# Optimization experiments

Measured on AMD Instinct MI355X. Metric: run time of the kernel, lower is better.

Reference implementation:

```python
import jax, jax.numpy as jnp
import numpy as np

N, E, G = 100000, 1600000, 64   # nodes, edges, graphs
IN, H, OUT = 32, 128, 3


def setup_inputs() -> dict:
    key = jax.random.key(0)
    ks = jax.random.split(key, 24)
    def w(k, i, o):
        return (jax.random.normal(k, (i, o), jnp.float32) / np.sqrt(i)).astype(jnp.float32)
    inp = {
        "x": jax.random.normal(ks[0], (N, IN), jnp.float32),
        "edge_index": jax.random.randint(ks[1], (2, E), 0, N, dtype=jnp.int32).astype(jnp.int64),
        "batch": jnp.sort(jax.random.randint(ks[2], (N,), 0, G, dtype=jnp.int32)).astype(jnp.int64),
        # SAGEConv layer 0 (in->hidden): lin_l (neighbors, with bias), lin_r (root, no bias)
        "Wl0": w(ks[3], IN, H), "bl0": jnp.zeros((H,), jnp.float32), "Wr0": w(ks[4], IN, H),
        # SAGEConv layers 1,2 (hidden->hidden)
        "Wl1": w(ks[5], H, H), "bl1": jnp.zeros((H,), jnp.float32), "Wr1": w(ks[6], H, H),
        "Wl2": w(ks[7], H, H), "bl2": jnp.zeros((H,), jnp.float32), "Wr2": w(ks[8], H, H),
        # output head
        "Wfc": w(ks[9], H, OUT), "bfc": jnp.zeros((OUT,), jnp.float32),
        # aux MLP on (dim1, dim3)
        "Wa1": w(ks[10], 2, H), "ba1": jnp.zeros((H,), jnp.float32),
        "Wa2": w(ks[11], H, H), "ba2": jnp.zeros((H,), jnp.float32),
        "Wao": w(ks[12], H, 1), "bao": jnp.zeros((1,), jnp.float32),
    }
    return inp


def _sage_conv(x, src, dst, Wl, bl, Wr):
    # PyG SAGEConv (mean aggr): out = lin_l(mean_{j in N(i)} x_j) + lin_r(x_i)
    msg = x[src]                                   # [E, d] gather
    agg = jax.ops.segment_sum(msg, dst, num_segments=N)
    cnt = jax.ops.segment_sum(jnp.ones((src.shape[0],), x.dtype), dst, num_segments=N)
    mean = agg / jnp.maximum(cnt, 1.0)[:, None]
    return mean @ Wl + bl + x @ Wr


def reference(x, edge_index, batch,
              Wl0, bl0, Wr0, Wl1, bl1, Wr1, Wl2, bl2, Wr2,
              Wfc, bfc, Wa1, ba1, Wa2, ba2, Wao, bao):
    src, dst = edge_index[0], edge_index[1]
    h = jax.nn.relu(_sage_conv(x, src, dst, Wl0, bl0, Wr0))   # dropout is identity in eval
    h = jax.nn.relu(_sage_conv(h, src, dst, Wl1, bl1, Wr1))
    h = jax.nn.relu(_sage_conv(h, src, dst, Wl2, bl2, Wr2))
    main = h @ Wfc + bfc                                      # [N, 3]
    dim1, dim3 = main[:, 0], main[:, 2]
    aux_in = jnp.stack([dim1, dim3], axis=-1)                 # [N, 2]
    a = jax.nn.relu(aux_in @ Wa1 + ba1)
    a = jax.nn.relu(a @ Wa2 + ba2)
    aux_out = (a @ Wao + bao)[:, 0]                           # [N]
    final = jnp.stack([dim1, aux_out, dim3], axis=-1)         # [N, 3]
    # global mean pool over graph ids
    s = jax.ops.segment_sum(final, batch, num_segments=G)
    c = jax.ops.segment_sum(jnp.ones((final.shape[0],), final.dtype), batch, num_segments=G)
    return s / jnp.maximum(c, 1.0)[:, None]                   # [G, 3]
```

## Files before the change

kernel.cpp:

```cpp
#include <hip/hip_runtime.h>

#define NR 128
#define PART_CH 4096
typedef unsigned short ushortT;
typedef __attribute__((ext_vector_type(8))) short short8;
typedef __attribute__((ext_vector_type(4))) float float4v;
typedef __attribute__((ext_vector_type(2))) float float2v;

__device__ __forceinline__ unsigned short f32_to_bf16_rne(float f) {
    unsigned u = __float_as_uint(f);
    unsigned r = (u + 0x7fffu + ((u >> 16) & 1u)) >> 16;
    return (unsigned short)r;
}

__device__ __forceinline__ unsigned char f32_to_fp8(float f) {
    return (unsigned char)(__builtin_amdgcn_cvt_pk_fp8_f32(f, f, 0, false) & 0xff);
}

__device__ __forceinline__ void accum8(float* acc, uint4 v) {
    unsigned u[4] = {v.x, v.y, v.z, v.w};
#pragma unroll
    for (int q = 0; q < 4; q++) {
        acc[2 * q]     += __uint_as_float(u[q] << 16);
        acc[2 * q + 1] += __uint_as_float(u[q] & 0xffff0000u);
    }
}

__device__ __forceinline__ void accum16_fp8(float* acc, uint4 v) {
    unsigned u[4] = {v.x, v.y, v.z, v.w};
#pragma unroll
    for (int q = 0; q < 4; q++) {
        float2v lo = __builtin_amdgcn_cvt_pk_f32_fp8(u[q], false);
        float2v hi = __builtin_amdgcn_cvt_pk_f32_fp8(u[q], true);
        acc[4 * q + 0] += lo.x;
        acc[4 * q + 1] += lo.y;
        acc[4 * q + 2] += hi.x;
        acc[4 * q + 3] += hi.y;
    }
}


__launch_bounds__(256)
__global__ void bucket_count(const int* __restrict__ dst, int* __restrict__ bcnt, int E, int NB) {
    __shared__ int h[1024];
    int t = threadIdx.x;
    for (int j = t; j < NB; j += 256) h[j] = 0;
    __syncthreads();
    int e0 = blockIdx.x * PART_CH;
    int e1 = min(e0 + PART_CH, E);
    for (int base = e0; base < e1; base += 2048) {
        int idx = base + t;
        int d[8];
        int cnt = 0;
#pragma unroll
        for (int u = 0; u < 8; u++) {
            int e = idx + u * 256;
            if (e < e1) d[cnt++] = dst[e];
        }
        for (int u = 0; u < cnt; u++) atomicAdd(&h[d[u] >> 7], 1);
    }
    __syncthreads();
    for (int j = t; j < NB; j += 256) {
        int v = h[j];
        if (v) atomicAdd(&bcnt[j], v);
    }
}

__launch_bounds__(256)
__global__ void bucket_scan(const int* __restrict__ bcnt, int* __restrict__ bstart,
                            int* __restrict__ gcur, int NB, int E) {
    __shared__ int sh[256];
    int t = threadIdx.x;
    int v[4];
    int tot = 0;
#pragma unroll
    for (int j = 0; j < 4; j++) {
        int idx = t * 4 + j;
        v[j] = (idx < NB) ? bcnt[idx] : 0;
        tot += v[j];
    }
    sh[t] = tot;
    __syncthreads();
    for (int off = 1; off < 256; off <<= 1) {
        int add = (t >= off) ? sh[t - off] : 0;
        __syncthreads();
        sh[t] += add;
        __syncthreads();
    }
    int run = sh[t] - tot;
#pragma unroll
    for (int j = 0; j < 4; j++) {
        int idx = t * 4 + j;
        if (idx < NB) { bstart[idx] = run; gcur[idx] = run; }
        run += v[j];
    }
    if (t == 0) bstart[NB] = E;
}

__launch_bounds__(256)
__global__ void partition_edges(const int* __restrict__ src, const int* __restrict__ dst,
                                int* __restrict__ gcur, unsigned* __restrict__ packed,
                                int E, int NB) {
    __shared__ int hist[1024];
    __shared__ int base[1024];
    int t = threadIdx.x;
    int e0 = blockIdx.x * PART_CH;
    int e1 = min(e0 + PART_CH, E);
    for (int j = t; j < NB; j += 256) hist[j] = 0;
    __syncthreads();
    for (int bb = e0; bb < e1; bb += 2048) {
        int idx = bb + t;
        int d[8];
        int cnt = 0;
#pragma unroll
        for (int u = 0; u < 8; u++) {
            int e = idx + u * 256;
            if (e < e1) d[cnt++] = dst[e];
        }
        for (int u = 0; u < cnt; u++) atomicAdd(&hist[d[u] >> 7], 1);
    }
    __syncthreads();
    for (int j = t; j < NB; j += 256) {
        int h = hist[j];
        base[j] = h ? atomicAdd(&gcur[j], h) : 0;
    }
    __syncthreads();
    for (int j = t; j < NB; j += 256) hist[j] = base[j];
    __syncthreads();
    for (int bb = e0; bb < e1; bb += 2048) {
        int idx = bb + t;
        int d[8], s[8];
        int cnt = 0;
#pragma unroll
        for (int u = 0; u < 8; u++) {
            int e = idx + u * 256;
            if (e < e1) { d[cnt] = dst[e]; s[cnt] = src[e]; cnt++; }
        }
        for (int u = 0; u < cnt; u++) {
            int dd = d[u];
            int pos = atomicAdd(&hist[dd >> 7], 1);
            packed[pos] = (unsigned)s[u] | ((unsigned)(dd & (NR - 1)) << 17);
        }
    }
}

__launch_bounds__(256)
__global__ void bucket_sort(const unsigned* __restrict__ packed, const int* __restrict__ bstart,
                            int* __restrict__ row_start, int* __restrict__ srcs, int N) {
    __shared__ int cnt[NR];
    __shared__ int sc[NR];
    __shared__ int cur[NR];
    int b = blockIdx.x, t = threadIdx.x;
    int nb0 = b * NR;
    int nnode = min(NR, N - nb0);
    int lo = bstart[b], hi = bstart[b + 1];
    if (t < NR) cnt[t] = 0;
    __syncthreads();
    for (int bb = lo; bb < hi; bb += 2048) {
        int idx = bb + t;
        unsigned pk[8];
        int c = 0;
#pragma unroll
        for (int u = 0; u < 8; u++) {
            int e = idx + u * 256;
            if (e < hi) pk[c++] = packed[e];
        }
        for (int u = 0; u < c; u++) atomicAdd(&cnt[pk[u] >> 17], 1);
    }
    __syncthreads();
    if (t < NR) sc[t] = cnt[t];
    __syncthreads();
    for (int off = 1; off < NR; off <<= 1) {
        int add = (t >= off && t < NR) ? sc[t - off] : 0;
        __syncthreads();
        if (t < NR) sc[t] += add;
        __syncthreads();
    }
    if (t < nnode) {
        int s = lo + sc[t] - cnt[t];
        row_start[nb0 + t] = s;
        cur[t] = s;
    }
    if (t == 0 && nb0 + nnode == N) row_start[N] = hi;
    __syncthreads();
    for (int bb = lo; bb < hi; bb += 2048) {
        int idx = bb + t;
        unsigned pk[8];
        int c = 0;
#pragma unroll
        for (int u = 0; u < 8; u++) {
            int e = idx + u * 256;
            if (e < hi) pk[c++] = packed[e];
        }
        for (int u = 0; u < c; u++) {
            int pos = atomicAdd(&cur[pk[u] >> 17], 1);
            srcs[pos] = (int)(pk[u] & 0x1FFFFu);
        }
    }
}


__global__ void prep_fused(const float* __restrict__ x, ushortT* __restrict__ xbf, int n4,
                           const float* __restrict__ Wl0, const float* __restrict__ Wr0,
                           const float* __restrict__ Wl1, const float* __restrict__ Wr1,
                           const float* __restrict__ Wl2, const float* __restrict__ Wr2,
                           const float* __restrict__ Wa2,
                           ushortT* __restrict__ Wt0, ushortT* __restrict__ Wt1,
                           ushortT* __restrict__ Wt2, ushortT* __restrict__ Wa2t) {
    int tid0 = blockIdx.x * 256 + threadIdx.x;
    if (tid0 < n4) {
        float4 v = ((const float4*)x)[tid0];
        ushort4 o;
        o.x = f32_to_bf16_rne(v.x);
        o.y = f32_to_bf16_rne(v.y);
        o.z = f32_to_bf16_rne(v.z);
        o.w = f32_to_bf16_rne(v.w);
        ((ushort4*)xbf)[tid0] = o;
        return;
    }
    int tid = tid0 - n4;
    if (tid < 8192) {
        int col = tid >> 6, k = tid & 63;
        float v = (k < 32) ? Wl0[k * 128 + col] : Wr0[(k - 32) * 128 + col];
        Wt0[col * 64 + ((k + 8 * col) & 63)] = f32_to_bf16_rne(v);
    } else if (tid < 8192 + 32768) {
        int j = tid - 8192;
        int col = j >> 8, k = j & 255;
        float v = (k < 128) ? Wl1[k * 128 + col] : Wr1[(k - 128) * 128 + col];
        Wt1[col * 256 + ((k + 8 * col) & 255)] = f32_to_bf16_rne(v);
    } else if (tid < 8192 + 65536) {
        int j = tid - 8192 - 32768;
        int col = j >> 8, k = j & 255;
        float v = (k < 128) ? Wl2[k * 128 + col] : Wr2[(k - 128) * 128 + col];
        Wt2[col * 256 + ((k + 8 * col) & 255)] = f32_to_bf16_rne(v);
    } else if (tid < 8192 + 65536 + 16384) {
        int j = tid - 8192 - 65536;
        int col = j >> 7, k = j & 127;
        Wa2t[col * 128 + ((k + 8 * col) & 127)] = f32_to_bf16_rne(Wa2[k * 128 + col]);
    }
}


template <int CPN>
__launch_bounds__(256)
__global__ void aggregate_mean_bf16(const uint4* __restrict__ hin, ushortT* __restrict__ out,
                                    const int* __restrict__ srcs, const int* __restrict__ rs, int n) {
    constexpr int TPN = CPN / 2;
    int tid = blockIdx.x * 256 + threadIdx.x;
    if (tid >= n * TPN) return;
    int i = tid / TPN;
    int c = tid & (TPN - 1);
    int lo = rs[i], hi = rs[i + 1];
    float acc0[8], acc1[8];
#pragma unroll
    for (int q = 0; q < 8; q++) { acc0[q] = 0.f; acc1[q] = 0.f; }
    int e = lo;
    for (; e + 8 <= hi; e += 8) {
        int s[8];
#pragma unroll
        for (int u = 0; u < 8; u++) s[u] = srcs[e + u];
        uint4 va[8], vb[8];
#pragma unroll
        for (int u = 0; u < 8; u++) {
            va[u] = hin[(size_t)s[u] * CPN + c];
            vb[u] = hin[(size_t)s[u] * CPN + c + TPN];
        }
#pragma unroll
        for (int u = 0; u < 8; u++) { accum8(acc0, va[u]); accum8(acc1, vb[u]); }
    }
    for (; e < hi; ++e) {
        int s = srcs[e];
        accum8(acc0, hin[(size_t)s * CPN + c]);
        accum8(acc1, hin[(size_t)s * CPN + c + TPN]);
    }
    float inv = 1.0f / (float)max(hi - lo, 1);
    uint4 o0, o1;
    o0.x = (unsigned)f32_to_bf16_rne(acc0[0] * inv) | ((unsigned)f32_to_bf16_rne(acc0[1] * inv) << 16);
    o0.y = (unsigned)f32_to_bf16_rne(acc0[2] * inv) | ((unsigned)f32_to_bf16_rne(acc0[3] * inv) << 16);
    o0.z = (unsigned)f32_to_bf16_rne(acc0[4] * inv) | ((unsigned)f32_to_bf16_rne(acc0[5] * inv) << 16);
    o0.w = (unsigned)f32_to_bf16_rne(acc0[6] * inv) | ((unsigned)f32_to_bf16_rne(acc0[7] * inv) << 16);
    o1.x = (unsigned)f32_to_bf16_rne(acc1[0] * inv) | ((unsigned)f32_to_bf16_rne(acc1[1] * inv) << 16);
    o1.y = (unsigned)f32_to_bf16_rne(acc1[2] * inv) | ((unsigned)f32_to_bf16_rne(acc1[3] * inv) << 16);
    o1.z = (unsigned)f32_to_bf16_rne(acc1[4] * inv) | ((unsigned)f32_to_bf16_rne(acc1[5] * inv) << 16);
    o1.w = (unsigned)f32_to_bf16_rne(acc1[6] * inv) | ((unsigned)f32_to_bf16_rne(acc1[7] * inv) << 16);
    ((uint4*)out)[(size_t)i * CPN + c] = o0;
    ((uint4*)out)[(size_t)i * CPN + c + TPN] = o1;
}


__launch_bounds__(256)
__global__ void aggregate_mean_fp8(const uint4* __restrict__ hin, ushortT* __restrict__ out,
                                   const int* __restrict__ srcs, const int* __restrict__ rs, int n) {
    int tid = blockIdx.x * 256 + threadIdx.x;
    if (tid >= n * 8) return;
    int i = tid >> 3;
    int c = tid & 7;
    int lo = rs[i], hi = rs[i + 1];
    float acc[16];
#pragma unroll
    for (int q = 0; q < 16; q++) acc[q] = 0.f;
    int e = lo;
    for (; e + 8 <= hi; e += 8) {
        int s[8];
#pragma unroll
        for (int u = 0; u < 8; u++) s[u] = srcs[e + u];
        uint4 v[8];
#pragma unroll
        for (int u = 0; u < 8; u++) v[u] = hin[(size_t)s[u] * 8 + c];
#pragma unroll
        for (int u = 0; u < 8; u++) accum16_fp8(acc, v[u]);
    }
    for (; e + 4 <= hi; e += 4) {
        int s[4];
#pragma unroll
        for (int u = 0; u < 4; u++) s[u] = srcs[e + u];
        uint4 v[4];
#pragma unroll
        for (int u = 0; u < 4; u++) v[u] = hin[(size_t)s[u] * 8 + c];
#pragma unroll
        for (int u = 0; u < 4; u++) accum16_fp8(acc, v[u]);
    }
    for (; e < hi; ++e) accum16_fp8(acc, hin[(size_t)srcs[e] * 8 + c]);
    float inv = 1.0f / (float)max(hi - lo, 1);
    uint4 o0, o1;
    o0.x = (unsigned)f32_to_bf16_rne(acc[0] * inv)  | ((unsigned)f32_to_bf16_rne(acc[1] * inv) << 16);
    o0.y = (unsigned)f32_to_bf16_rne(acc[2] * inv)  | ((unsigned)f32_to_bf16_rne(acc[3] * inv) << 16);
    o0.z = (unsigned)f32_to_bf16_rne(acc[4] * inv)  | ((unsigned)f32_to_bf16_rne(acc[5] * inv) << 16);
    o0.w = (unsigned)f32_to_bf16_rne(acc[6] * inv)  | ((unsigned)f32_to_bf16_rne(acc[7] * inv) << 16);
    o1.x = (unsigned)f32_to_bf16_rne(acc[8] * inv)  | ((unsigned)f32_to_bf16_rne(acc[9] * inv) << 16);
    o1.y = (unsigned)f32_to_bf16_rne(acc[10] * inv) | ((unsigned)f32_to_bf16_rne(acc[11] * inv) << 16);
    o1.z = (unsigned)f32_to_bf16_rne(acc[12] * inv) | ((unsigned)f32_to_bf16_rne(acc[13] * inv) << 16);
    o1.w = (unsigned)f32_to_bf16_rne(acc[14] * inv) | ((unsigned)f32_to_bf16_rne(acc[15] * inv) << 16);
    ((uint4*)out)[(size_t)i * 16 + c * 2]     = o0;
    ((uint4*)out)[(size_t)i * 16 + c * 2 + 1] = o1;
}


template <int KH, bool OUT_BF16, bool OUT_FP8>
__launch_bounds__(256, 2)
__global__ void gemm_mfma(const ushortT* __restrict__ Am, const ushortT* __restrict__ Ah,
                          const ushortT* __restrict__ Wt, const float* __restrict__ bias,
                          float* __restrict__ outf, ushortT* __restrict__ outbf,
                          unsigned char* __restrict__ outf8, int n) {
    constexpr int KT = 2 * KH;
    __shared__ ushortT sW[128 * KT];
    int t = threadIdx.x;
    constexpr int TOT16 = 128 * KT * 2 / 16;
    {
        const uint4* Wg = (const uint4*)Wt;
        uint4* Ws = (uint4*)sW;
        for (int j = t; j < TOT16; j += 256) Ws[j] = Wg[j];
    }
    __syncthreads();
    int wv = t >> 6, lane = t & 63;
    int q = lane >> 4, cid = lane & 15;
    int rbase = blockIdx.x * 128 + wv * 32;
    int r0 = rbase + cid, r1 = r0 + 16;
    int r0c = min(r0, n - 1), r1c = min(r1, n - 1);
    float4v acc[2][8];
#pragma unroll
    for (int i = 0; i < 2; i++)
#pragma unroll
        for (int j = 0; j < 8; j++) acc[i][j] = (float4v){0.f, 0.f, 0.f, 0.f};
    int swz = q * 8 + 8 * cid;
#pragma unroll
    for (int ks = 0; ks < KT / 32; ++ks) {
        int kk = ks * 32;
        const ushortT* abase = (kk < KH) ? Am : Ah;
        int kc = (kk < KH) ? kk : kk - KH;
        short8 a0 = *(const short8*)(abase + (size_t)r0c * KH + kc + q * 8);
        short8 a1 = *(const short8*)(abase + (size_t)r1c * KH + kc + q * 8);
#pragma unroll
        for (int j = 0; j < 8; ++j) {
            int col = j * 16 + cid;
            int p = (kk + swz + j * 128) & (KT - 1);
            short8 b = *(const short8*)(sW + col * KT + p);
            acc[0][j] = __builtin_amdgcn_mfma_f32_16x16x32_bf16(a0, b, acc[0][j], 0, 0, 0);
            acc[1][j] = __builtin_amdgcn_mfma_f32_16x16x32_bf16(a1, b, acc[1][j], 0, 0, 0);
        }
    }
    float bo[8];
#pragma unroll
    for (int j = 0; j < 8; ++j) bo[j] = bias[j * 16 + cid];
#pragma unroll
    for (int i = 0; i < 2; ++i) {
#pragma unroll
        for (int rr = 0; rr < 4; ++rr) {
            int row = rbase + i * 16 + q * 4 + rr;
            if (row < n) {
#pragma unroll
                for (int j = 0; j < 8; ++j) {
                    int col = j * 16 + cid;
                    float v = fmaxf(acc[i][j][rr] + bo[j], 0.f);
                    if (OUT_BF16) outbf[(size_t)row * 128 + col] = f32_to_bf16_rne(v);
                    if (OUT_FP8)  outf8[(size_t)row * 128 + col] = f32_to_fp8(v);
                    if (!OUT_BF16 && !OUT_FP8) outf[(size_t)row * 128 + col] = v;
                }
            }
        }
    }
}


template <int KH>
__launch_bounds__(256, 2)
__global__ void gemm_mfma_fin(const ushortT* __restrict__ Am, const ushortT* __restrict__ Ah,
                              const ushortT* __restrict__ Wt, const float* __restrict__ bias,
                              const float* __restrict__ Wfc, const float* __restrict__ bfc,
                              float* __restrict__ fin, int n) {
    constexpr int KT = 2 * KH;
    __shared__ ushortT sW[128 * KT];
    int t = threadIdx.x;
    constexpr int TOT16 = 128 * KT * 2 / 16;
    {
        const uint4* Wg = (const uint4*)Wt;
        uint4* Ws = (uint4*)sW;
        for (int j = t; j < TOT16; j += 256) Ws[j] = Wg[j];
    }
    __syncthreads();
    int wv = t >> 6, lane = t & 63;
    int q = lane >> 4, cid = lane & 15;
    int rbase = blockIdx.x * 128 + wv * 32;
    int r0 = rbase + cid, r1 = r0 + 16;
    int r0c = min(r0, n - 1), r1c = min(r1, n - 1);
    float4v acc[2][8];
#pragma unroll
    for (int i = 0; i < 2; i++)
#pragma unroll
        for (int j = 0; j < 8; j++) acc[i][j] = (float4v){0.f, 0.f, 0.f, 0.f};
    int swz = q * 8 + 8 * cid;
#pragma unroll
    for (int ks = 0; ks < KT / 32; ++ks) {
        int kk = ks * 32;
        const ushortT* abase = (kk < KH) ? Am : Ah;
        int kc = (kk < KH) ? kk : kk - KH;
        short8 a0 = *(const short8*)(abase + (size_t)r0c * KH + kc + q * 8);
        short8 a1 = *(const short8*)(abase + (size_t)r1c * KH + kc + q * 8);
#pragma unroll
        for (int j = 0; j < 8; ++j) {
            int col = j * 16 + cid;
            int p = (kk + swz + j * 128) & (KT - 1);
            short8 b = *(const short8*)(sW + col * KT + p);
            acc[0][j] = __builtin_amdgcn_mfma_f32_16x16x32_bf16(a0, b, acc[0][j], 0, 0, 0);
            acc[1][j] = __builtin_amdgcn_mfma_f32_16x16x32_bf16(a1, b, acc[1][j], 0, 0, 0);
        }
    }
    float bo[8], w1[8], w3[8];
#pragma unroll
    for (int j = 0; j < 8; ++j) {
        int col = j * 16 + cid;
        bo[j] = bias[col];
        w1[j] = Wfc[col * 3 + 0];
        w3[j] = Wfc[col * 3 + 2];
    }
    float bfc0 = bfc[0], bfc2 = bfc[2];
#pragma unroll
    for (int i = 0; i < 2; ++i) {
#pragma unroll
        for (int rr = 0; rr < 4; ++rr) {
            float p1 = 0.f, p3 = 0.f;
#pragma unroll
            for (int j = 0; j < 8; ++j) {
                float v = fmaxf(acc[i][j][rr] + bo[j], 0.f);
                p1 += v * w1[j];
                p3 += v * w3[j];
            }
            p1 += __shfl_xor(p1, 1, 64); p3 += __shfl_xor(p3, 1, 64);
            p1 += __shfl_xor(p1, 2, 64); p3 += __shfl_xor(p3, 2, 64);
            p1 += __shfl_xor(p1, 4, 64); p3 += __shfl_xor(p3, 4, 64);
            p1 += __shfl_xor(p1, 8, 64); p3 += __shfl_xor(p3, 8, 64);
            int row = rbase + i * 16 + q * 4 + rr;
            if (cid == 0 && row < n) {
                fin[(size_t)row * 3 + 0] = p1 + bfc0;
                fin[(size_t)row * 3 + 2] = p3 + bfc2;
            }
        }
    }
}


__launch_bounds__(256, 4)
__global__ void head_mfma(const ushortT* __restrict__ Wa2t, const float* __restrict__ Wa1,
                          const float* __restrict__ ba1, const float* __restrict__ ba2,
                          const float* __restrict__ Wao, const float* __restrict__ bao,
                          float* __restrict__ fin, int n) {
    __shared__ ushortT sW[128 * 128];
    __shared__ float sD1[128], sD3[128];
    __shared__ float sWa1a[128], sWa1b[128], sBa1[128];
    int t = threadIdx.x;
    {
        const uint4* Wg = (const uint4*)Wa2t;
        uint4* Ws = (uint4*)sW;
        for (int j = t; j < 2048; j += 256) Ws[j] = Wg[j];
    }
    int rbase = blockIdx.x * 128;
    if (t < 128) {
        sWa1a[t] = Wa1[t];
        sWa1b[t] = Wa1[128 + t];
        sBa1[t] = ba1[t];
        int row = min(rbase + t, n - 1);
        sD1[t] = fin[(size_t)row * 3 + 0];
        sD3[t] = fin[(size_t)row * 3 + 2];
    }
    __syncthreads();
    int wv = t >> 6, lane = t & 63;
    int q = lane >> 4, cid = lane & 15;
    int rl0 = wv * 32 + cid, rl1 = rl0 + 16;
    float d1a = sD1[rl0], d3a = sD3[rl0];
    float d1b = sD1[rl1], d3b = sD3[rl1];
    float4v acc[2][8];
#pragma unroll
    for (int i = 0; i < 2; i++)
#pragma unroll
        for (int j = 0; j < 8; j++) acc[i][j] = (float4v){0.f, 0.f, 0.f, 0.f};
    int swz = q * 8 + 8 * cid;
#pragma unroll
    for (int ks = 0; ks < 4; ++ks) {
        int k0 = ks * 32 + q * 8;
        short8 a0, a1;
#pragma unroll
        for (int j = 0; j < 8; ++j) {
            int k = k0 + j;
            float w0 = sWa1a[k], w1 = sWa1b[k], bb = sBa1[k];
            float v0 = fmaxf(fmaf(d1a, w0, fmaf(d3a, w1, bb)), 0.f);
            float v1 = fmaxf(fmaf(d1b, w0, fmaf(d3b, w1, bb)), 0.f);
            a0[j] = (short)f32_to_bf16_rne(v0);
            a1[j] = (short)f32_to_bf16_rne(v1);
        }
        int p = (ks * 32 + swz) & 127;
#pragma unroll
        for (int j = 0; j < 8; ++j) {
            short8 b = *(const short8*)(sW + (j * 16 + cid) * 128 + p);
            acc[0][j] = __builtin_amdgcn_mfma_f32_16x16x32_bf16(a0, b, acc[0][j], 0, 0, 0);
            acc[1][j] = __builtin_amdgcn_mfma_f32_16x16x32_bf16(a1, b, acc[1][j], 0, 0, 0);
        }
    }
    float b2[8], wo[8];
#pragma unroll
    for (int j = 0; j < 8; ++j) {
        int col = j * 16 + cid;
        b2[j] = ba2[col];
        wo[j] = Wao[col];
    }
    float bao0 = bao[0];
#pragma unroll
    for (int i = 0; i < 2; ++i) {
#pragma unroll
        for (int rr = 0; rr < 4; ++rr) {
            float s = 0.f;
#pragma unroll
            for (int j = 0; j < 8; ++j) s += fmaxf(acc[i][j][rr] + b2[j], 0.f) * wo[j];
            s += __shfl_xor(s, 1, 64);
            s += __shfl_xor(s, 2, 64);
            s += __shfl_xor(s, 4, 64);
            s += __shfl_xor(s, 8, 64);
            int row = rbase + wv * 32 + i * 16 + q * 4 + rr;
            if (cid == 0 && row < n) fin[(size_t)row * 3 + 1] = s + bao0;
        }
    }
}


__global__ void pool_kernel(const float* __restrict__ fin, const int* __restrict__ batch,
                            float* __restrict__ out, int n) {
    int g = blockIdx.x, t = threadIdx.x;
    int lo = 0, hi = n;
    while (lo < hi) { int mid = (lo + hi) >> 1; if (batch[mid] < g) lo = mid + 1; else hi = mid; }
    int start = lo;
    lo = 0; hi = n;
    while (lo < hi) { int mid = (lo + hi) >> 1; if (batch[mid] < g + 1) lo = mid + 1; else hi = mid; }
    int end = lo;
    float s0 = 0.f, s1 = 0.f, s2 = 0.f;
    for (int i = start + t; i < end; i += 256) {
        s0 += fin[(size_t)i * 3 + 0];
        s1 += fin[(size_t)i * 3 + 1];
        s2 += fin[(size_t)i * 3 + 2];
    }
    __shared__ float r0[256], r1[256], r2[256];
    r0[t] = s0; r1[t] = s1; r2[t] = s2;
    __syncthreads();
    for (int off = 128; off > 0; off >>= 1) {
        if (t < off) { r0[t] += r0[t + off]; r1[t] += r1[t + off]; r2[t] += r2[t + off]; }
        __syncthreads();
    }
    if (t == 0) {
        float c = (float)max(end - start, 1);
        out[g * 3 + 0] = r0[0] / c;
        out[g * 3 + 1] = r1[0] / c;
        out[g * 3 + 2] = r2[0] / c;
    }
}


extern "C" void kernel_launch(void* const* d_in, const int* in_sizes, int n_in,
                              void* d_out, int out_size, void* d_ws, size_t ws_size,
                              hipStream_t stream) {
    const float* x    = (const float*)d_in[0];
    const int*   ei   = (const int*)d_in[1];
    const int*   batch= (const int*)d_in[2];
    const float* Wl0  = (const float*)d_in[3];
    const float* bl0  = (const float*)d_in[4];
    const float* Wr0  = (const float*)d_in[5];
    const float* Wl1  = (const float*)d_in[6];
    const float* bl1  = (const float*)d_in[7];
    const float* Wr1  = (const float*)d_in[8];
    const float* Wl2  = (const float*)d_in[9];
    const float* bl2  = (const float*)d_in[10];
    const float* Wr2  = (const float*)d_in[11];
    const float* Wfc  = (const float*)d_in[12];
    const float* bfc  = (const float*)d_in[13];
    const float* Wa1  = (const float*)d_in[14];
    const float* ba1  = (const float*)d_in[15];
    const float* Wa2  = (const float*)d_in[16];
    const float* ba2  = (const float*)d_in[17];
    const float* Wao  = (const float*)d_in[18];
    const float* bao  = (const float*)d_in[19];

    const int N = in_sizes[0] / 32;
    const int E = in_sizes[1] / 2;
    const int G = out_size / 3;
    const int* src = ei;
    const int* dst = ei + E;
    float* out = (float*)d_out;
    const int NB = (N + NR - 1) / NR;

    char* p = (char*)d_ws;
    auto carve = [&](size_t bytes) {
        void* r = (void*)p;
        p += (bytes + 255) & ~(size_t)255;
        return r;
    };
    int*           bcnt     = (int*)carve((size_t)NB * 4);
    int*           bstart   = (int*)carve((size_t)(NB + 1) * 4);
    int*           gcur     = (int*)carve((size_t)NB * 4);
    int*           row_start= (int*)carve((size_t)(N + 1) * 4);
    unsigned*      packed   = (unsigned*)carve((size_t)E * 4);
    int*           srcs     = (int*)carve((size_t)E * 4);
    ushortT*       aggbf    = (ushortT*)carve((size_t)N * 128 * 2);
    ushortT*       xbf      = (ushortT*)carve((size_t)N * 32 * 2);
    ushortT*       hbf0     = (ushortT*)carve((size_t)N * 128 * 2);
    ushortT*       hbf1     = (ushortT*)carve((size_t)N * 128 * 2);
    unsigned char* hf8_0    = (unsigned char*)carve((size_t)N * 128);
    unsigned char* hf8_1    = (unsigned char*)carve((size_t)N * 128);
    float*         fin      = (float*)carve((size_t)N * 3 * 4);
    ushortT*       Wt0      = (ushortT*)carve((size_t)128 * 64 * 2);
    ushortT*       Wt1      = (ushortT*)carve((size_t)128 * 256 * 2);
    ushortT*       Wt2      = (ushortT*)carve((size_t)128 * 256 * 2);
    ushortT*       Wa2t     = (ushortT*)carve((size_t)128 * 128 * 2);

    const int gemm_grid = (N + 127) / 128;
    const int part_grid = (E + PART_CH - 1) / PART_CH;
    const int n4 = N * 32 / 4;

    prep_fused<<<(n4 + 90112 + 255) / 256, 256, 0, stream>>>(
        x, xbf, n4, Wl0, Wr0, Wl1, Wr1, Wl2, Wr2, Wa2, Wt0, Wt1, Wt2, Wa2t);

    hipMemsetAsync(bcnt, 0, (size_t)NB * 4, stream);
    bucket_count<<<part_grid, 256, 0, stream>>>(dst, bcnt, E, NB);
    bucket_scan<<<1, 256, 0, stream>>>(bcnt, bstart, gcur, NB, E);
    partition_edges<<<part_grid, 256, 0, stream>>>(src, dst, gcur, packed, E, NB);
    bucket_sort<<<NB, 256, 0, stream>>>(packed, bstart, row_start, srcs, N);

    aggregate_mean_bf16<4><<<(N * 2 + 255) / 256, 256, 0, stream>>>(
        (const uint4*)xbf, aggbf, srcs, row_start, N);
    gemm_mfma<32, true, true><<<gemm_grid, 256, 0, stream>>>(
        aggbf, xbf, Wt0, bl0, (float*)nullptr, hbf0, hf8_0, N);
    aggregate_mean_fp8<<<(N * 8 + 255) / 256, 256, 0, stream>>>(
        (const uint4*)hf8_0, aggbf, srcs, row_start, N);
    gemm_mfma<128, true, true><<<gemm_grid, 256, 0, stream>>>(
        aggbf, hbf0, Wt1, bl1, (float*)nullptr, hbf1, hf8_1, N);
    aggregate_mean_fp8<<<(N * 8 + 255) / 256, 256, 0, stream>>>(
        (const uint4*)hf8_1, aggbf, srcs, row_start, N);
    gemm_mfma_fin<128><<<gemm_grid, 256, 0, stream>>>(
        aggbf, hbf1, Wt2, bl2, Wfc, bfc, fin, N);

    head_mfma<<<gemm_grid, 256, 0, stream>>>(
        Wa2t, Wa1, ba1, ba2, Wao, bao, fin, N);

    pool_kernel<<<G, 256, 0, stream>>>(fin, batch, out, N);
}
```

Measured before the change: 358.0 us.

## Fuse fp8 neighbor aggregation into GEMM via LDS and merge prep with bucket count

Layers 1 and 2 now compute the mean aggregation per 128-row tile directly into a swizzled LDS buffer and feed it to the MFMA GEMM in the same kernel. This drops the bf16 aggregate round trip through global memory and two launches. The weight matrix is read from global or L2 instead of being staged in LDS. Separately, the input/weight prep kernel and the bucket-count kernel are merged into one launch using a block-index split. This trades more load on each GEMM block (gather latency, lower occupancy) for less memory traffic.

```diff
diff --git a/kernel.cpp b/kernel.cpp
--- a/kernel.cpp
+++ b/kernel.cpp
@@ -41,173 +41,41 @@
 
 
 __launch_bounds__(256)
-__global__ void bucket_count(const int* __restrict__ dst, int* __restrict__ bcnt, int E, int NB) {
-    __shared__ int h[1024];
-    int t = threadIdx.x;
-    for (int j = t; j < NB; j += 256) h[j] = 0;
-    __syncthreads();
-    int e0 = blockIdx.x * PART_CH;
-    int e1 = min(e0 + PART_CH, E);
-    for (int base = e0; base < e1; base += 2048) {
-        int idx = base + t;
-        int d[8];
-        int cnt = 0;
-#pragma unroll
-        for (int u = 0; u < 8; u++) {
-            int e = idx + u * 256;
-            if (e < e1) d[cnt++] = dst[e];
-        }
-        for (int u = 0; u < cnt; u++) atomicAdd(&h[d[u] >> 7], 1);
-    }
-    __syncthreads();
-    for (int j = t; j < NB; j += 256) {
-        int v = h[j];
-        if (v) atomicAdd(&bcnt[j], v);
-    }
-}
-
-__launch_bounds__(256)
-__global__ void bucket_scan(const int* __restrict__ bcnt, int* __restrict__ bstart,
-                            int* __restrict__ gcur, int NB, int E) {
-    __shared__ int sh[256];
-    int t = threadIdx.x;
-    int v[4];
-    int tot = 0;
-#pragma unroll
-    for (int j = 0; j < 4; j++) {
-        int idx = t * 4 + j;
-        v[j] = (idx < NB) ? bcnt[idx] : 0;
-        tot += v[j];
-    }
-    sh[t] = tot;
-    __syncthreads();
-    for (int off = 1; off < 256; off <<= 1) {
-        int add = (t >= off) ? sh[t - off] : 0;
-        __syncthreads();
-        sh[t] += add;
-        __syncthreads();
-    }
-    int run = sh[t] - tot;
-#pragma unroll
-    for (int j = 0; j < 4; j++) {
-        int idx = t * 4 + j;
-        if (idx < NB) { bstart[idx] = run; gcur[idx] = run; }
-        run += v[j];
-    }
-    if (t == 0) bstart[NB] = E;
-}
-
-__launch_bounds__(256)
-__global__ void partition_edges(const int* __restrict__ src, const int* __restrict__ dst,
-                                int* __restrict__ gcur, unsigned* __restrict__ packed,
-                                int E, int NB) {
-    __shared__ int hist[1024];
-    __shared__ int base[1024];
-    int t = threadIdx.x;
-    int e0 = blockIdx.x * PART_CH;
-    int e1 = min(e0 + PART_CH, E);
-    for (int j = t; j < NB; j += 256) hist[j] = 0;
-    __syncthreads();
-    for (int bb = e0; bb < e1; bb += 2048) {
-        int idx = bb + t;
-        int d[8];
-        int cnt = 0;
-#pragma unroll
-        for (int u = 0; u < 8; u++) {
-            int e = idx + u * 256;
-            if (e < e1) d[cnt++] = dst[e];
-        }
-        for (int u = 0; u < cnt; u++) atomicAdd(&hist[d[u] >> 7], 1);
-    }
-    __syncthreads();
-    for (int j = t; j < NB; j += 256) {
-        int h = hist[j];
-        base[j] = h ? atomicAdd(&gcur[j], h) : 0;
-    }
-    __syncthreads();
-    for (int j = t; j < NB; j += 256) hist[j] = base[j];
-    __syncthreads();
-    for (int bb = e0; bb < e1; bb += 2048) {
-        int idx = bb + t;
-        int d[8], s[8];
-        int cnt = 0;
-#pragma unroll
-        for (int u = 0; u < 8; u++) {
-            int e = idx + u * 256;
-            if (e < e1) { d[cnt] = dst[e]; s[cnt] = src[e]; cnt++; }
-        }
-        for (int u = 0; u < cnt; u++) {
-            int dd = d[u];
-            int pos = atomicAdd(&hist[dd >> 7], 1);
-            packed[pos] = (unsigned)s[u] | ((unsigned)(dd & (NR - 1)) << 17);
-        }
-    }
-}
-
-__launch_bounds__(256)
-__global__ void bucket_sort(const unsigned* __restrict__ packed, const int* __restrict__ bstart,
-                            int* __restrict__ row_start, int* __restrict__ srcs, int N) {
-    __shared__ int cnt[NR];
-    __shared__ int sc[NR];
-    __shared__ int cur[NR];
-    int b = blockIdx.x, t = threadIdx.x;
-    int nb0 = b * NR;
-    int nnode = min(NR, N - nb0);
-    int lo = bstart[b], hi = bstart[b + 1];
-    if (t < NR) cnt[t] = 0;
-    __syncthreads();
-    for (int bb = lo; bb < hi; bb += 2048) {
-        int idx = bb + t;
-        unsigned pk[8];
-        int c = 0;
-#pragma unroll
-        for (int u = 0; u < 8; u++) {
-            int e = idx + u * 256;
-            if (e < hi) pk[c++] = packed[e];
-        }
-        for (int u = 0; u < c; u++) atomicAdd(&cnt[pk[u] >> 17], 1);
-    }
-    __syncthreads();
-    if (t < NR) sc[t] = cnt[t];
-    __syncthreads();
-    for (int off = 1; off < NR; off <<= 1) {
-        int add = (t >= off && t < NR) ? sc[t - off] : 0;
-        __syncthreads();
-        if (t < NR) sc[t] += add;
-        __syncthreads();
-    }
-    if (t < nnode) {
-        int s = lo + sc[t] - cnt[t];
-        row_start[nb0 + t] = s;
-        cur[t] = s;
-    }
-    if (t == 0 && nb0 + nnode == N) row_start[N] = hi;
-    __syncthreads();
-    for (int bb = lo; bb < hi; bb += 2048) {
-        int idx = bb + t;
-        unsigned pk[8];
-        int c = 0;
-#pragma unroll
-        for (int u = 0; u < 8; u++) {
-            int e = idx + u * 256;
-            if (e < hi) pk[c++] = packed[e];
-        }
-        for (int u = 0; u < c; u++) {
-            int pos = atomicAdd(&cur[pk[u] >> 17], 1);
-            srcs[pos] = (int)(pk[u] & 0x1FFFFu);
-        }
-    }
-}
-
-
-__global__ void prep_fused(const float* __restrict__ x, ushortT* __restrict__ xbf, int n4,
+__global__ void prep_count(const float* __restrict__ x, ushortT* __restrict__ xbf, int n4, int nprep,
                            const float* __restrict__ Wl0, const float* __restrict__ Wr0,
                            const float* __restrict__ Wl1, const float* __restrict__ Wr1,
                            const float* __restrict__ Wl2, const float* __restrict__ Wr2,
                            const float* __restrict__ Wa2,
                            ushortT* __restrict__ Wt0, ushortT* __restrict__ Wt1,
-                           ushortT* __restrict__ Wt2, ushortT* __restrict__ Wa2t) {
-    int tid0 = blockIdx.x * 256 + threadIdx.x;
+                           ushortT* __restrict__ Wt2, ushortT* __restrict__ Wa2t,
+                           const int* __restrict__ dst, int* __restrict__ bcnt, int E, int NB) {
+    __shared__ int h[1024];
+    int t = threadIdx.x;
+    if ((int)blockIdx.x >= nprep) {
+        int blk = blockIdx.x - nprep;
+        for (int j = t; j < NB; j += 256) h[j] = 0;
+        __syncthreads();
+        int e0 = blk * PART_CH;
+        int e1 = min(e0 + PART_CH, E);
+        for (int base = e0; base < e1; base += 2048) {
+            int idx = base + t;
+            int d[8];
+            int cnt = 0;
+#pragma unroll
+            for (int u = 0; u < 8; u++) {
+                int e = idx + u * 256;
+                if (e < e1) d[cnt++] = dst[e];
+            }
+            for (int u = 0; u < cnt; u++) atomicAdd(&h[d[u] >> 7], 1);
+        }
+        __syncthreads();
+        for (int j = t; j < NB; j += 256) {
+            int v = h[j];
+            if (v) atomicAdd(&bcnt[j], v);
+        }
+        return;
+    }
+    int tid0 = blockIdx.x * 256 + t;
     if (tid0 < n4) {
         float4 v = ((const float4*)x)[tid0];
         ushort4 o;
@@ -241,6 +109,140 @@
 }
 
 
+__launch_bounds__(256)
+__global__ void bucket_scan(const int* __restrict__ bcnt, int* __restrict__ bstart,
+                            int* __restrict__ gcur, int NB, int E) {
+    __shared__ int sh[256];
+    int t = threadIdx.x;
+    int v[4];
+    int tot = 0;
+#pragma unroll
+    for (int j = 0; j < 4; j++) {
+        int idx = t * 4 + j;
+        v[j] = (idx < NB) ? bcnt[idx] : 0;
+        tot += v[j];
+    }
+    sh[t] = tot;
+    __syncthreads();
+    for (int off = 1; off < 256; off <<= 1) {
+        int add = (t >= off) ? sh[t - off] : 0;
+        __syncthreads();
+        sh[t] += add;
+        __syncthreads();
+    }
+    int run = sh[t] - tot;
+#pragma unroll
+    for (int j = 0; j < 4; j++) {
+        int idx = t * 4 + j;
+        if (idx < NB) { bstart[idx] = run; gcur[idx] = run; }
+        run += v[j];
+    }
+    if (t == 0) bstart[NB] = E;
+}
+
+__launch_bounds__(256)
+__global__ void partition_edges(const int* __restrict__ src, const int* __restrict__ dst,
+                                int* __restrict__ gcur, unsigned* __restrict__ packed,
+                                int E, int NB) {
+    __shared__ int hist[1024];
+    __shared__ int base[1024];
+    int t = threadIdx.x;
+    int e0 = blockIdx.x * PART_CH;
+    int e1 = min(e0 + PART_CH, E);
+    for (int j = t; j < NB; j += 256) hist[j] = 0;
+    __syncthreads();
+    for (int bb = e0; bb < e1; bb += 2048) {
+        int idx = bb + t;
+        int d[8];
+        int cnt = 0;
+#pragma unroll
+        for (int u = 0; u < 8; u++) {
+            int e = idx + u * 256;
+            if (e < e1) d[cnt++] = dst[e];
+        }
+        for (int u = 0; u < cnt; u++) atomicAdd(&hist[d[u] >> 7], 1);
+    }
+    __syncthreads();
+    for (int j = t; j < NB; j += 256) {
+        int h = hist[j];
+        base[j] = h ? atomicAdd(&gcur[j], h) : 0;
+    }
+    __syncthreads();
+    for (int j = t; j < NB; j += 256) hist[j] = base[j];
+    __syncthreads();
+    for (int bb = e0; bb < e1; bb += 2048) {
+        int idx = bb + t;
+        int d[8], s[8];
+        int cnt = 0;
+#pragma unroll
+        for (int u = 0; u < 8; u++) {
+            int e = idx + u * 256;
+            if (e < e1) { d[cnt] = dst[e]; s[cnt] = src[e]; cnt++; }
+        }
+        for (int u = 0; u < cnt; u++) {
+            int dd = d[u];
+            int pos = atomicAdd(&hist[dd >> 7], 1);
+            packed[pos] = (unsigned)s[u] | ((unsigned)(dd & (NR - 1)) << 17);
+        }
+    }
+}
+
+__launch_bounds__(256)
+__global__ void bucket_sort(const unsigned* __restrict__ packed, const int* __restrict__ bstart,
+                            int* __restrict__ row_start, int* __restrict__ srcs, int N) {
+    __shared__ int cnt[NR];
+    __shared__ int sc[NR];
+    __shared__ int cur[NR];
+    int b = blockIdx.x, t = threadIdx.x;
+    int nb0 = b * NR;
+    int nnode = min(NR, N - nb0);
+    int lo = bstart[b], hi = bstart[b + 1];
+    if (t < NR) cnt[t] = 0;
+    __syncthreads();
+    for (int bb = lo; bb < hi; bb += 2048) {
+        int idx = bb + t;
+        unsigned pk[8];
+        int c = 0;
+#pragma unroll
+        for (int u = 0; u < 8; u++) {
+            int e = idx + u * 256;
+            if (e < hi) pk[c++] = packed[e];
+        }
+        for (int u = 0; u < c; u++) atomicAdd(&cnt[pk[u] >> 17], 1);
+    }
+    __syncthreads();
+    if (t < NR) sc[t] = cnt[t];
+    __syncthreads();
+    for (int off = 1; off < NR; off <<= 1) {
+        int add = (t >= off && t < NR) ? sc[t - off] : 0;
+        __syncthreads();
+        if (t < NR) sc[t] += add;
+        __syncthreads();
+    }
+    if (t < nnode) {
+        int s = lo + sc[t] - cnt[t];
+        row_start[nb0 + t] = s;
+        cur[t] = s;
+    }
+    if (t == 0 && nb0 + nnode == N) row_start[N] = hi;
+    __syncthreads();
+    for (int bb = lo; bb < hi; bb += 2048) {
+        int idx = bb + t;
+        unsigned pk[8];
+        int c = 0;
+#pragma unroll
+        for (int u = 0; u < 8; u++) {
+            int e = idx + u * 256;
+            if (e < hi) pk[c++] = packed[e];
+        }
+        for (int u = 0; u < c; u++) {
+            int pos = atomicAdd(&cur[pk[u] >> 17], 1);
+            srcs[pos] = (int)(pk[u] & 0x1FFFFu);
+        }
+    }
+}
+
+
 template <int CPN>
 __launch_bounds__(256)
 __global__ void aggregate_mean_bf16(const uint4* __restrict__ hin, ushortT* __restrict__ out,
@@ -285,54 +287,6 @@
     o1.w = (unsigned)f32_to_bf16_rne(acc1[6] * inv) | ((unsigned)f32_to_bf16_rne(acc1[7] * inv) << 16);
     ((uint4*)out)[(size_t)i * CPN + c] = o0;
     ((uint4*)out)[(size_t)i * CPN + c + TPN] = o1;
-}
-
-
-__launch_bounds__(256)
-__global__ void aggregate_mean_fp8(const uint4* __restrict__ hin, ushortT* __restrict__ out,
-                                   const int* __restrict__ srcs, const int* __restrict__ rs, int n) {
-    int tid = blockIdx.x * 256 + threadIdx.x;
-    if (tid >= n * 8) return;
-    int i = tid >> 3;
-    int c = tid & 7;
-    int lo = rs[i], hi = rs[i + 1];
-    float acc[16];
-#pragma unroll
-    for (int q = 0; q < 16; q++) acc[q] = 0.f;
-    int e = lo;
-    for (; e + 8 <= hi; e += 8) {
-        int s[8];
-#pragma unroll
-        for (int u = 0; u < 8; u++) s[u] = srcs[e + u];
-        uint4 v[8];
-#pragma unroll
-        for (int u = 0; u < 8; u++) v[u] = hin[(size_t)s[u] * 8 + c];
-#pragma unroll
-        for (int u = 0; u < 8; u++) accum16_fp8(acc, v[u]);
-    }
-    for (; e + 4 <= hi; e += 4) {
-        int s[4];
-#pragma unroll
-        for (int u = 0; u < 4; u++) s[u] = srcs[e + u];
-        uint4 v[4];
-#pragma unroll
-        for (int u = 0; u < 4; u++) v[u] = hin[(size_t)s[u] * 8 + c];
-#pragma unroll
-        for (int u = 0; u < 4; u++) accum16_fp8(acc, v[u]);
-    }
-    for (; e < hi; ++e) accum16_fp8(acc, hin[(size_t)srcs[e] * 8 + c]);
-    float inv = 1.0f / (float)max(hi - lo, 1);
-    uint4 o0, o1;
-    o0.x = (unsigned)f32_to_bf16_rne(acc[0] * inv)  | ((unsigned)f32_to_bf16_rne(acc[1] * inv) << 16);
-    o0.y = (unsigned)f32_to_bf16_rne(acc[2] * inv)  | ((unsigned)f32_to_bf16_rne(acc[3] * inv) << 16);
-    o0.z = (unsigned)f32_to_bf16_rne(acc[4] * inv)  | ((unsigned)f32_to_bf16_rne(acc[5] * inv) << 16);
-    o0.w = (unsigned)f32_to_bf16_rne(acc[6] * inv)  | ((unsigned)f32_to_bf16_rne(acc[7] * inv) << 16);
-    o1.x = (unsigned)f32_to_bf16_rne(acc[8] * inv)  | ((unsigned)f32_to_bf16_rne(acc[9] * inv) << 16);
-    o1.y = (unsigned)f32_to_bf16_rne(acc[10] * inv) | ((unsigned)f32_to_bf16_rne(acc[11] * inv) << 16);
-    o1.z = (unsigned)f32_to_bf16_rne(acc[12] * inv) | ((unsigned)f32_to_bf16_rne(acc[13] * inv) << 16);
-    o1.w = (unsigned)f32_to_bf16_rne(acc[14] * inv) | ((unsigned)f32_to_bf16_rne(acc[15] * inv) << 16);
-    ((uint4*)out)[(size_t)i * 16 + c * 2]     = o0;
-    ((uint4*)out)[(size_t)i * 16 + c * 2 + 1] = o1;
 }
 
 
@@ -402,27 +356,63 @@
 }
 
 
-template <int KH>
-__launch_bounds__(256, 2)
-__global__ void gemm_mfma_fin(const ushortT* __restrict__ Am, const ushortT* __restrict__ Ah,
-                              const ushortT* __restrict__ Wt, const float* __restrict__ bias,
-                              const float* __restrict__ Wfc, const float* __restrict__ bfc,
-                              float* __restrict__ fin, int n) {
-    constexpr int KT = 2 * KH;
-    __shared__ ushortT sW[128 * KT];
+template <bool FIN>
+__launch_bounds__(256, 3)
+__global__ void fused_agg_gemm(const uint4* __restrict__ hf8in, const ushortT* __restrict__ Hbf,
+                               const ushortT* __restrict__ Wt, const float* __restrict__ bias,
+                               ushortT* __restrict__ outbf, unsigned char* __restrict__ outf8,
+                               const float* __restrict__ Wfc, const float* __restrict__ bfc,
+                               float* __restrict__ fin,
+                               const int* __restrict__ srcs, const int* __restrict__ rs, int n) {
+    __shared__ ushortT sA[128 * 128];
     int t = threadIdx.x;
-    constexpr int TOT16 = 128 * KT * 2 / 16;
-    {
-        const uint4* Wg = (const uint4*)Wt;
-        uint4* Ws = (uint4*)sW;
-        for (int j = t; j < TOT16; j += 256) Ws[j] = Wg[j];
+    int rbase = blockIdx.x * 128;
+#pragma unroll
+    for (int it = 0; it < 4; ++it) {
+        int r = it * 32 + (t >> 3);
+        int c = t & 7;
+        int node = min(rbase + r, n - 1);
+        int lo = rs[node], hi = rs[node + 1];
+        float acc[16];
+#pragma unroll
+        for (int qq = 0; qq < 16; qq++) acc[qq] = 0.f;
+        int e = lo;
+        for (; e + 8 <= hi; e += 8) {
+            int s[8];
+#pragma unroll
+            for (int u = 0; u < 8; u++) s[u] = srcs[e + u];
+            uint4 v[8];
+#pragma unroll
+            for (int u = 0; u < 8; u++) v[u] = hf8in[(size_t)s[u] * 8 + c];
+#pragma unroll
+            for (int u = 0; u < 8; u++) accum16_fp8(acc, v[u]);
+        }
+        for (; e + 4 <= hi; e += 4) {
+            int s[4];
+#pragma unroll
+            for (int u = 0; u < 4; u++) s[u] = srcs[e + u];
+            uint4 v[4];
+#pragma unroll
+            for (int u = 0; u < 4; u++) v[u] = hf8in[(size_t)s[u] * 8 + c];
+#pragma unroll
+            for (int u = 0; u < 4; u++) accum16_fp8(acc, v[u]);
+        }
+        for (; e < hi; ++e) accum16_fp8(acc, hf8in[(size_t)srcs[e] * 8 + c]);
+        float inv = 1.0f / (float)max(hi - lo, 1);
+        unsigned o[8];
+#pragma unroll
+        for (int qq = 0; qq < 8; qq++)
+            o[qq] = (unsigned)f32_to_bf16_rne(acc[2 * qq] * inv)
+                  | ((unsigned)f32_to_bf16_rne(acc[2 * qq + 1] * inv) << 16);
+        int sw = r & 15;
+        *(uint4*)(sA + r * 128 + ((2 * c) ^ sw) * 8)     = make_uint4(o[0], o[1], o[2], o[3]);
+        *(uint4*)(sA + r * 128 + ((2 * c + 1) ^ sw) * 8) = make_uint4(o[4], o[5], o[6], o[7]);
     }
     __syncthreads();
     int wv = t >> 6, lane = t & 63;
     int q = lane >> 4, cid = lane & 15;
-    int rbase = blockIdx.x * 128 + wv * 32;
-    int r0 = rbase + cid, r1 = r0 + 16;
-    int r0c = min(r0, n - 1), r1c = min(r1, n - 1);
+    int rl = wv * 32 + cid;
+    int r0c = min(rbase + rl, n - 1), r1c = min(rbase + rl + 16, n - 1);
     float4v acc[2][8];
 #pragma unroll
     for (int i = 0; i < 2; i++)
@@ -430,49 +420,75 @@
         for (int j = 0; j < 8; j++) acc[i][j] = (float4v){0.f, 0.f, 0.f, 0.f};
     int swz = q * 8 + 8 * cid;
 #pragma unroll
-    for (int ks = 0; ks < KT / 32; ++ks) {
-        int kk = ks * 32;
-        const ushortT* abase = (kk < KH) ? Am : Ah;
-        int kc = (kk < KH) ? kk : kk - KH;
-        short8 a0 = *(const short8*)(abase + (size_t)r0c * KH + kc + q * 8);
-        short8 a1 = *(const short8*)(abase + (size_t)r1c * KH + kc + q * 8);
+    for (int ks = 0; ks < 8; ++ks) {
+        short8 a0, a1;
+        if (ks < 4) {
+            int ch = ((ks * 4 + q) ^ (rl & 15)) * 8;
+            a0 = *(const short8*)(sA + rl * 128 + ch);
+            a1 = *(const short8*)(sA + (rl + 16) * 128 + ch);
+        } else {
+            int kc = (ks - 4) * 32 + q * 8;
+            a0 = *(const short8*)(Hbf + (size_t)r0c * 128 + kc);
+            a1 = *(const short8*)(Hbf + (size_t)r1c * 128 + kc);
+        }
+#pragma unroll
+        for (int j = 0; j < 8; ++j) {
+            int p = (ks * 32 + swz + j * 128) & 255;
+            short8 b = *(const short8*)(Wt + (size_t)(j * 16 + cid) * 256 + p);
+            acc[0][j] = __builtin_amdgcn_mfma_f32_16x16x32_bf16(a0, b, acc[0][j], 0, 0, 0);
+            acc[1][j] = __builtin_amdgcn_mfma_f32_16x16x32_bf16(a1, b, acc[1][j], 0, 0, 0);
+        }
+    }
+    if (!FIN) {
+        float bo[8];
+#pragma unroll
+        for (int j = 0; j < 8; ++j) bo[j] = bias[j * 16 + cid];
+#pragma unroll
+        for (int i = 0; i < 2; ++i) {
+#pragma unroll
+            for (int rr = 0; rr < 4; ++rr) {
+                int row = rbase + wv * 32 + i * 16 + q * 4 + rr;
+                if (row < n) {
+#pragma unroll
+                    for (int j = 0; j < 8; ++j) {
+                        int col = j * 16 + cid;
+                        float v = fmaxf(acc[i][j][rr] + bo[j], 0.f);
+                        outbf[(size_t)row * 128 + col] = f32_to_bf16_rne(v);
+                        outf8[(size_t)row * 128 + col] = f32_to_fp8(v);
+                    }
+                }
+            }
+        }
+    } else {
+        float bo[8], w1[8], w3[8];
 #pragma unroll
         for (int j = 0; j < 8; ++j) {
             int col = j * 16 + cid;
-            int p = (kk + swz + j * 128) & (KT - 1);
-            short8 b = *(const short8*)(sW + col * KT + p);
-            acc[0][j] = __builtin_amdgcn_mfma_f32_16x16x32_bf16(a0, b, acc[0][j], 0, 0, 0);
-            acc[1][j] = __builtin_amdgcn_mfma_f32_16x16x32_bf16(a1, b, acc[1][j], 0, 0, 0);
-        }
-    }
-    float bo[8], w1[8], w3[8];
-#pragma unroll
-    for (int j = 0; j < 8; ++j) {
-        int col = j * 16 + cid;
-        bo[j] = bias[col];
-        w1[j] = Wfc[col * 3 + 0];
-        w3[j] = Wfc[col * 3 + 2];
-    }
-    float bfc0 = bfc[0], bfc2 = bfc[2];
-#pragma unroll
-    for (int i = 0; i < 2; ++i) {
-#pragma unroll
-        for (int rr = 0; rr < 4; ++rr) {
-            float p1 = 0.f, p3 = 0.f;
-#pragma unroll
-            for (int j = 0; j < 8; ++j) {
-                float v = fmaxf(acc[i][j][rr] + bo[j], 0.f);
-                p1 += v * w1[j];
-                p3 += v * w3[j];
-            }
-            p1 += __shfl_xor(p1, 1, 64); p3 += __shfl_xor(p3, 1, 64);
-            p1 += __shfl_xor(p1, 2, 64); p3 += __shfl_xor(p3, 2, 64);
-            p1 += __shfl_xor(p1, 4, 64); p3 += __shfl_xor(p3, 4, 64);
-            p1 += __shfl_xor(p1, 8, 64); p3 += __shfl_xor(p3, 8, 64);
-            int row = rbase + i * 16 + q * 4 + rr;
-            if (cid == 0 && row < n) {
-                fin[(size_t)row * 3 + 0] = p1 + bfc0;
-                fin[(size_t)row * 3 + 2] = p3 + bfc2;
+            bo[j] = bias[col];
+            w1[j] = Wfc[col * 3 + 0];
+            w3[j] = Wfc[col * 3 + 2];
+        }
+        float bfc0 = bfc[0], bfc2 = bfc[2];
+#pragma unroll
+        for (int i = 0; i < 2; ++i) {
+#pragma unroll
+            for (int rr = 0; rr < 4; ++rr) {
+                float p1 = 0.f, p3 = 0.f;
+#pragma unroll
+                for (int j = 0; j < 8; ++j) {
+                    float v = fmaxf(acc[i][j][rr] + bo[j], 0.f);
+                    p1 += v * w1[j];
+                    p3 += v * w3[j];
+                }
+                p1 += __shfl_xor(p1, 1, 64); p3 += __shfl_xor(p3, 1, 64);
+                p1 += __shfl_xor(p1, 2, 64); p3 += __shfl_xor(p3, 2, 64);
+                p1 += __shfl_xor(p1, 4, 64); p3 += __shfl_xor(p3, 4, 64);
+                p1 += __shfl_xor(p1, 8, 64); p3 += __shfl_xor(p3, 8, 64);
+                int row = rbase + wv * 32 + i * 16 + q * 4 + rr;
+                if (cid == 0 && row < n) {
+                    fin[(size_t)row * 3 + 0] = p1 + bfc0;
+                    fin[(size_t)row * 3 + 2] = p3 + bfc2;
+                }
             }
         }
     }
@@ -636,7 +652,7 @@
     int*           row_start= (int*)carve((size_t)(N + 1) * 4);
     unsigned*      packed   = (unsigned*)carve((size_t)E * 4);
     int*           srcs     = (int*)carve((size_t)E * 4);
-    ushortT*       aggbf    = (ushortT*)carve((size_t)N * 128 * 2);
+    ushortT*       aggbf    = (ushortT*)carve((size_t)N * 32 * 2);
     ushortT*       xbf      = (ushortT*)carve((size_t)N * 32 * 2);
     ushortT*       hbf0     = (ushortT*)carve((size_t)N * 128 * 2);
     ushortT*       hbf1     = (ushortT*)carve((size_t)N * 128 * 2);
@@ -651,12 +667,13 @@
     const int gemm_grid = (N + 127) / 128;
     const int part_grid = (E + PART_CH - 1) / PART_CH;
     const int n4 = N * 32 / 4;
-
-    prep_fused<<<(n4 + 90112 + 255) / 256, 256, 0, stream>>>(
-        x, xbf, n4, Wl0, Wr0, Wl1, Wr1, Wl2, Wr2, Wa2, Wt0, Wt1, Wt2, Wa2t);
+    const int nprep = (n4 + 90112 + 255) / 256;
 
     hipMemsetAsync(bcnt, 0, (size_t)NB * 4, stream);
-    bucket_count<<<part_grid, 256, 0, stream>>>(dst, bcnt, E, NB);
+    prep_count<<<nprep + part_grid, 256, 0, stream>>>(
+        x, xbf, n4, nprep, Wl0, Wr0, Wl1, Wr1, Wl2, Wr2, Wa2,
+        Wt0, Wt1, Wt2, Wa2t, dst, bcnt, E, NB);
+
     bucket_scan<<<1, 256, 0, stream>>>(bcnt, bstart, gcur, NB, E);
     partition_edges<<<part_grid, 256, 0, stream>>>(src, dst, gcur, packed, E, NB);
     bucket_sort<<<NB, 256, 0, stream>>>(packed, bstart, row_start, srcs, N);
@@ -665,14 +682,14 @@
         (const uint4*)xbf, aggbf, srcs, row_start, N);
     gemm_mfma<32, true, true><<<gemm_grid, 256, 0, stream>>>(
         aggbf, xbf, Wt0, bl0, (float*)nullptr, hbf0, hf8_0, N);
-    aggregate_mean_fp8<<<(N * 8 + 255) / 256, 256, 0, stream>>>(
-        (const uint4*)hf8_0, aggbf, srcs, row_start, N);
-    gemm_mfma<128, true, true><<<gemm_grid, 256, 0, stream>>>(
-        aggbf, hbf0, Wt1, bl1, (float*)nullptr, hbf1, hf8_1, N);
-    aggregate_mean_fp8<<<(N * 8 + 255) / 256, 256, 0, stream>>>(
-        (const uint4*)hf8_1, aggbf, srcs, row_start, N);
-    gemm_mfma_fin<128><<<gemm_grid, 256, 0, stream>>>(
-        aggbf, hbf1, Wt2, bl2, Wfc, bfc, fin, N);
+
+    fused_agg_gemm<false><<<gemm_grid, 256, 0, stream>>>(
+        (const uint4*)hf8_0, hbf0, Wt1, bl1, hbf1, hf8_1,
+        (const float*)nullptr, (const float*)nullptr, (float*)nullptr,
+        srcs, row_start, N);
+    fused_agg_gemm<true><<<gemm_grid, 256, 0, stream>>>(
+        (const uint4*)hf8_1, hbf1, Wt2, bl2, (ushortT*)nullptr, (unsigned char*)nullptr,
+        Wfc, bfc, fin, srcs, row_start, N);
 
     head_mfma<<<gemm_grid, 256, 0, stream>>>(
         Wa2t, Wa1, ba1, ba2, Wao, bao, fin, N);
```

Result: slower. 371.5 us (+3.8%).
